# Kernel tuning notes

Hardware: AMD Instinct MI355X
Metric: run time of the kernel (lower is better)

Reference implementation:

```python
import jax, jax.numpy as jnp
import numpy as np

V, E, H, L = 32000, 512, 1024, 2
B, S, T = 32, 64, 64


def setup_inputs() -> dict:
    key = jax.random.key(0)
    ks = jax.random.split(key, 16)
    sd = 0.05
    p = lambda k, shape: (jax.random.normal(k, shape, jnp.float32) * sd)
    z = lambda shape: jnp.zeros(shape, jnp.float32)
    return {
        "tgt_batch": jax.random.randint(ks[0], (B, S), 0, V),
        "enc_h": p(ks[1], (L, B, H)),
        "enc_c": p(ks[2], (L, B, H)),
        "enc_outputs": p(ks[3], (T, B, H)),
        "emb": p(ks[4], (V, E)),
        "W_ih0": p(ks[5], (4 * H, E + H)),
        "W_hh0": p(ks[6], (4 * H, H)),
        "b_ih0": z((4 * H,)),
        "b_hh0": z((4 * H,)),
        "W_ih1": p(ks[7], (4 * H, H)),
        "W_hh1": p(ks[8], (4 * H, H)),
        "b_ih1": z((4 * H,)),
        "b_hh1": z((4 * H,)),
        "Wa": p(ks[9], (H, 2 * H)),
        "ba": z((H,)),
        "va": p(ks[10], (H,)),
        "Wc": p(ks[11], (H, 2 * H)),
        "bc": z((H,)),
        "Wo": p(ks[12], (V, H)),
        "bo": z((V,)),
        "teacher_forcing": 1,
    }


def _lstm_cell(x, h, c, Wih, Whh, bih, bhh):
    # PyTorch gate order: i, f, g, o
    g = x @ Wih.T + bih + h @ Whh.T + bhh
    i, f, gg, o = jnp.split(g, 4, axis=1)
    c2 = jax.nn.sigmoid(f) * c + jax.nn.sigmoid(i) * jnp.tanh(gg)
    return jax.nn.sigmoid(o) * jnp.tanh(c2), c2


def reference(tgt_batch, enc_h, enc_c, enc_outputs, emb,
              W_ih0, W_hh0, b_ih0, b_hh0, W_ih1, W_hh1, b_ih1, b_hh1,
              Wa, ba, va, Wc, bc, Wo, bo, teacher_forcing):
    # teacher_forcing == 1 -> always feed the gold previous word (matches
    # the torch loop, whose sampling branch is never taken at tf=1.0).
    tgt = tgt_batch.T  # [S, B], seq-first

    def step(carry, x_t):
        h, c, attn_h = carry  # h,c: [L,B,H]; attn_h: [B,H]
        x = jnp.concatenate([emb[x_t], attn_h], axis=1)  # [B, E+H]
        h0, c0 = _lstm_cell(x, h[0], c[0], W_ih0, W_hh0, b_ih0, b_hh0)
        h1, c1 = _lstm_cell(h0, h[1], c[1], W_ih1, W_hh1, b_ih1, b_hh1)
        # additive ('concat') attention over encoder states, query = top h
        hid = jnp.broadcast_to(h1[None], enc_outputs.shape)  # [T,B,H]
        energy = jnp.tanh(jnp.concatenate([hid, enc_outputs], axis=-1) @ Wa.T + ba)
        scores = jnp.einsum('tbh,h->bt', energy, va)  # [B,T]
        weights = jax.nn.softmax(scores, axis=1)
        context = jnp.einsum('bt,tbh->bh', weights, enc_outputs)  # [B,H]
        attn_h2 = jnp.tanh(jnp.concatenate([h1, context], axis=1) @ Wc.T + bc)
        logp = jax.nn.log_softmax(attn_h2 @ Wo.T + bo, axis=1)  # [B,V]
        return (jnp.stack([h0, h1]), jnp.stack([c0, c1]), attn_h2), logp

    init = (enc_h, enc_c, jnp.zeros((tgt.shape[1], H), enc_h.dtype))
    _, dec_outputs = jax.lax.scan(step, init, tgt[:-1])  # [S-1, B, V]
    dec_output_words = jnp.argmax(dec_outputs, axis=-1).astype(jnp.int32)
    return dec_outputs, dec_output_words
```

## Files before the change

### kernel.cpp

```cpp
#include <hip/hip_runtime.h>
#include <math.h>

#define VOCAB 32000
#define EMBD  512
#define HID   1024
#define BATCH 32
#define SEQ   64
#define TENC  64
#define NSTEP 63
#define G4    4096

typedef __attribute__((ext_vector_type(8))) short short8;
typedef __attribute__((ext_vector_type(4))) float f32x4;
typedef __attribute__((ext_vector_type(4))) unsigned short us4;
typedef unsigned short u16;

__device__ __forceinline__ float4 ld4(const float* p) {
  return *reinterpret_cast<const float4*>(p);
}
__device__ __forceinline__ u16 f2bf(float x) {
  unsigned u = __float_as_uint(x);
  return (u16)((u + 0x7fffu + ((u >> 16) & 1u)) >> 16);
}
__device__ __forceinline__ float bf2f(u16 h) {
  return __uint_as_float(((unsigned)h) << 16);
}

template<int MODE>
__device__ __forceinline__ void mfma32(
    const u16* __restrict__ Xahi, const u16* __restrict__ Xalo,
    const u16* __restrict__ Xbhi, const u16* __restrict__ Xblo,
    const u16* __restrict__ Whi,  const u16* __restrict__ Wlo,
    int nt, float* res)
{
  const int tid = threadIdx.x;
  const int w = tid >> 6, l = tid & 63;
  const int c = l & 15, koct = l >> 4;
  constexpr int K   = (MODE == 0) ? 2048 : 1024;
  constexpr int WS  = (MODE == 0) ? 2048 : 1024;
  constexpr int SPW = K / 32 / 4;
  const int r0 = c, r1 = 16 + c;
  const int wr0 = (MODE == 0) ? ((r0 >> 3)*1024 + nt*8 + (r0 & 7)) : (nt*32 + r0);
  const int wr1 = (MODE == 0) ? ((r1 >> 3)*1024 + nt*8 + (r1 & 7)) : (nt*32 + r1);
  const u16* bh0 = Whi + (size_t)wr0 * WS;
  const u16* bh1 = Whi + (size_t)wr1 * WS;
  const u16* bl0 = Wlo + (size_t)wr0 * WS;
  const u16* bl1 = Wlo + (size_t)wr1 * WS;

  auto ldA = [&](int m, int kg, int lo) -> short8 {
    const u16* base;
    if (MODE == 0 && kg >= 1024) base = lo ? Xblo : Xbhi;
    else                         base = lo ? Xalo : Xahi;
    const int b = m*16 + c;
    return *reinterpret_cast<const short8*>(base + b*1024 + (kg & 1023));
  };

  f32x4 acc[2][2];
  #pragma unroll
  for (int m = 0; m < 2; ++m)
    #pragma unroll
    for (int n = 0; n < 2; ++n) acc[m][n] = (f32x4){0.f,0.f,0.f,0.f};

  const int s0 = w * SPW;
  short8 Ah[2], Al[2], Bh[2], Bl[2];
  {
    const int kg = s0*32 + koct*8;
    Ah[0]=ldA(0,kg,0); Ah[1]=ldA(1,kg,0); Al[0]=ldA(0,kg,1); Al[1]=ldA(1,kg,1);
    Bh[0]=*reinterpret_cast<const short8*>(bh0+kg);
    Bh[1]=*reinterpret_cast<const short8*>(bh1+kg);
    Bl[0]=*reinterpret_cast<const short8*>(bl0+kg);
    Bl[1]=*reinterpret_cast<const short8*>(bl1+kg);
  }
  for (int s = s0; s < s0 + SPW; ++s) {
    short8 nAh[2], nAl[2], nBh[2], nBl[2];
    if (s + 1 < s0 + SPW) {
      const int kg = (s+1)*32 + koct*8;
      nAh[0]=ldA(0,kg,0); nAh[1]=ldA(1,kg,0); nAl[0]=ldA(0,kg,1); nAl[1]=ldA(1,kg,1);
      nBh[0]=*reinterpret_cast<const short8*>(bh0+kg);
      nBh[1]=*reinterpret_cast<const short8*>(bh1+kg);
      nBl[0]=*reinterpret_cast<const short8*>(bl0+kg);
      nBl[1]=*reinterpret_cast<const short8*>(bl1+kg);
    }
    #pragma unroll
    for (int n = 0; n < 2; ++n)
      #pragma unroll
      for (int m = 0; m < 2; ++m) {
        acc[m][n] = __builtin_amdgcn_mfma_f32_16x16x32_bf16(Ah[m], Bh[n], acc[m][n], 0, 0, 0);
        acc[m][n] = __builtin_amdgcn_mfma_f32_16x16x32_bf16(Ah[m], Bl[n], acc[m][n], 0, 0, 0);
        acc[m][n] = __builtin_amdgcn_mfma_f32_16x16x32_bf16(Al[m], Bh[n], acc[m][n], 0, 0, 0);
      }
    #pragma unroll
    for (int i = 0; i < 2; ++i) { Ah[i]=nAh[i]; Al[i]=nAl[i]; Bh[i]=nBh[i]; Bl[i]=nBl[i]; }
  }
  #pragma unroll
  for (int m = 0; m < 2; ++m)
    #pragma unroll
    for (int n = 0; n < 2; ++n)
      #pragma unroll
      for (int r = 0; r < 4; ++r) {
        const int b = m*16 + koct*4 + r;
        const int rr = n*16 + c;
        res[w*1056 + b*33 + rr] = acc[m][n][r];
      }
}

struct GKM {
  const u16 *Xahi, *Xalo, *Xbhi, *Xblo;
  const u16 *Whi, *Wlo;
  const float* bsum; const float* gembt;
  float* c; u16 *hhi; u16 *hlo;
};

template<int HASGEMB>
__global__ __launch_bounds__(256) void gates_mfma_k(GKM P) {
  __shared__ float res[4*1056];
  mfma32<0>(P.Xahi, P.Xalo, P.Xbhi, P.Xblo, P.Whi, P.Wlo, blockIdx.x, res);
  __syncthreads();
  const int tid = threadIdx.x;
  const int b = tid >> 3, j = tid & 7;
  const int n = blockIdx.x*8 + j;
  float g4[4];
  #pragma unroll
  for (int g = 0; g < 4; ++g) {
    const int r = g*8 + j;
    float s = P.bsum[g*1024 + n]
            + res[b*33+r] + res[1056 + b*33+r] + res[2112 + b*33+r] + res[3168 + b*33+r];
    if (HASGEMB) s += P.gembt[(size_t)b*G4 + g*1024 + n];
    g4[g] = s;
  }
  const float si = 1.f/(1.f+expf(-g4[0]));
  const float sf = 1.f/(1.f+expf(-g4[1]));
  const float so = 1.f/(1.f+expf(-g4[3]));
  const int i = b*HID + n;
  const float cn = sf*P.c[i] + si*tanhf(g4[2]);
  P.c[i] = cn;
  const float h = so*tanhf(cn);
  const u16 hh = f2bf(h);
  P.hhi[i] = hh;
  P.hlo[i] = f2bf(h - bf2f(hh));
}

struct PKM {
  const u16 *Xhi, *Xlo; const u16 *Whi, *Wlo; float* Pq;
};

__global__ __launch_bounds__(256) void proj_mfma_k(PKM P) {
  __shared__ float res[4*1056];
  mfma32<1>(P.Xhi, P.Xlo, nullptr, nullptr, P.Whi, P.Wlo, blockIdx.x, res);
  __syncthreads();
  const int tid = threadIdx.x;
  #pragma unroll
  for (int q = 0; q < 4; ++q) {
    const int o = q*256 + tid;
    const int b = o >> 5, r = o & 31;
    const float s = res[b*33+r] + res[1056 + b*33+r]
                  + res[2112 + b*33+r] + res[3168 + b*33+r];
    P.Pq[(size_t)b*2048 + blockIdx.x*32 + r] = s;
  }
}

struct AKM {
  const float* Pq; const float* PreAC; const float* va; const float* bc;
  u16* AHthi; u16* AHtlo;
};

__global__ __launch_bounds__(1024) void attn_k(AKM P) {
  __shared__ float QS[HID];
  __shared__ float sw[TENC];
  __shared__ float W64[TENC];
  const int b = blockIdx.x;
  const int tid = threadIdx.x;
  QS[tid] = P.Pq[(size_t)b*2048 + tid];
  __syncthreads();
  const int lane = tid & 63, wid = tid >> 6;
  float vreg[16];
  #pragma unroll
  for (int i2 = 0; i2 < 16; ++i2) vreg[i2] = P.va[lane + 64*i2];
  #pragma unroll
  for (int j = 0; j < 4; ++j) {
    const int te = wid*4 + j;
    const float* pr = P.PreAC + ((size_t)te*BATCH + b)*2048;
    float s = 0.f;
    #pragma unroll
    for (int i2 = 0; i2 < 16; ++i2) {
      const int idx = lane + 64*i2;
      s += vreg[i2] * tanhf(QS[idx] + pr[idx]);
    }
    #pragma unroll
    for (int off = 32; off; off >>= 1) s += __shfl_xor(s, off);
    if (lane == 0) sw[te] = s;
  }
  __syncthreads();
  if (tid < TENC) {
    const float v = sw[tid];
    float mx = v;
    #pragma unroll
    for (int off = 32; off; off >>= 1) mx = fmaxf(mx, __shfl_xor(mx, off));
    const float e = expf(v - mx);
    float sum = e;
    #pragma unroll
    for (int off = 32; off; off >>= 1) sum += __shfl_xor(sum, off);
    W64[tid] = e / sum;
  }
  __syncthreads();
  const int hh = tid;
  float acc = 0.f;
  #pragma unroll 8
  for (int te = 0; te < TENC; ++te)
    acc += W64[te] * P.PreAC[((size_t)te*BATCH + b)*2048 + HID + hh];
  const float hc = P.Pq[(size_t)b*2048 + HID + hh] + P.bc[hh];
  const float ah = tanhf(acc + hc);
  const u16 ahh = f2bf(ah);
  P.AHthi[(size_t)b*HID + hh] = ahh;
  P.AHtlo[(size_t)b*HID + hh] = f2bf(ah - bf2f(ahh));
}

template<int MODE>
__global__ __launch_bounds__(256) void pack_k(const float* __restrict__ A,
                                              const float* __restrict__ B,
                                              u16* __restrict__ hi, u16* __restrict__ lo) {
  constexpr int ROWS = (MODE == 2) ? 2048 : 4096;
  constexpr int K    = (MODE == 2) ? 1024 : 2048;
  const size_t total = (size_t)ROWS * (K/4);
  for (size_t i = (size_t)blockIdx.x*256 + threadIdx.x; i < total;
       i += (size_t)gridDim.x*256) {
    const int row = (int)(i / (K/4));
    const int k = (int)(i % (K/4)) * 4;
    float4 v;
    if (MODE == 0) v = (k < 1024) ? ld4(A + (size_t)row*1536 + 512 + k)
                                  : ld4(B + (size_t)row*1024 + (k - 1024));
    else if (MODE == 1) v = (k < 1024) ? ld4(A + (size_t)row*1024 + k)
                                       : ld4(B + (size_t)row*1024 + (k - 1024));
    else v = (row < 1024) ? ld4(A + (size_t)row*2048 + k)
                          : ld4(B + (size_t)(row - 1024)*2048 + k);
    us4 h, l;
    h.x = f2bf(v.x); l.x = f2bf(v.x - bf2f(h.x));
    h.y = f2bf(v.y); l.y = f2bf(v.y - bf2f(h.y));
    h.z = f2bf(v.z); l.z = f2bf(v.z - bf2f(h.z));
    h.w = f2bf(v.w); l.w = f2bf(v.w - bf2f(h.w));
    *reinterpret_cast<us4*>(hi + i*4) = h;
    *reinterpret_cast<us4*>(lo + i*4) = l;
  }
}

__global__ __launch_bounds__(256) void cvt_k(const float* __restrict__ src,
                                             u16* __restrict__ hi,
                                             u16* __restrict__ lo, int n) {
  int i = (blockIdx.x*256 + threadIdx.x) * 4;
  const int stride = gridDim.x * 256 * 4;
  for (; i < n; i += stride) {
    const float4 v = ld4(src + i);
    us4 h, l;
    h.x = f2bf(v.x); l.x = f2bf(v.x - bf2f(h.x));
    h.y = f2bf(v.y); l.y = f2bf(v.y - bf2f(h.y));
    h.z = f2bf(v.z); l.z = f2bf(v.z - bf2f(h.z));
    h.w = f2bf(v.w); l.w = f2bf(v.w - bf2f(h.w));
    *reinterpret_cast<us4*>(hi + i) = h;
    *reinterpret_cast<us4*>(lo + i) = l;
  }
}

struct WGP {
  const float* A; const float* W; const float* W2; const float* bias;
  const int* tgt; const float* emb;
  float* C; int ldc;
};

template<int WM>
__device__ __forceinline__ float4 ldWL(const WGP& P, int r, int k) {
  if (WM == 2) return ld4(P.W + (size_t)r * (EMBD + HID) + k);
  if (r < HID) return ld4(P.W  + (size_t)r * (2*HID) + HID + k);
  return ld4(P.W2 + (size_t)(r - HID) * (2*HID) + HID + k);
}

template<int WM>
__device__ __forceinline__ float4 ldAL(const WGP& P, int row, int k) {
  if (WM == 2) {
    const int tok = P.tgt[(row & 31) * SEQ + (row >> 5)];
    return ld4(P.emb + (size_t)tok * EMBD + k);
  }
  return ld4(P.A + (size_t)row * 1024 + k);
}

template<int WM>
__global__ __launch_bounds__(256, 2) void gemmL(WGP P) {
  constexpr int KK = (WM == 2) ? 512 : 1024;
  __shared__ float At[32*36];
  __shared__ float Wt[32*260];
  const int tid = threadIdx.x;
  const int m0 = blockIdx.x * 32;
  const int n0 = blockIdx.y * 256;
  const int lr = tid >> 3, lc = (tid & 7) << 2;
  const int tn = tid & 31, tm = tid >> 5;
  float acc[4][8];
  #pragma unroll
  for (int i = 0; i < 4; ++i)
    #pragma unroll
    for (int x = 0; x < 8; ++x) acc[i][x] = 0.f;

  float4 av = ldAL<WM>(P, m0 + lr, lc);
  float4 wv[8];
  #pragma unroll
  for (int it = 0; it < 8; ++it) wv[it] = ldWL<WM>(P, n0 + lr + it*32, lc);

  for (int k0 = 0; k0 < KK; k0 += 32) {
    float4 avn, wvn[8];
    if (k0 + 32 < KK) {
      avn = ldAL<WM>(P, m0 + lr, k0 + 32 + lc);
      #pragma unroll
      for (int it = 0; it < 8; ++it) wvn[it] = ldWL<WM>(P, n0 + lr + it*32, k0 + 32 + lc);
    }
    __syncthreads();
    At[(lc+0)*36+lr]=av.x; At[(lc+1)*36+lr]=av.y; At[(lc+2)*36+lr]=av.z; At[(lc+3)*36+lr]=av.w;
    #pragma unroll
    for (int it = 0; it < 8; ++it) {
      const int r = lr + it*32;
      Wt[(lc+0)*260+r]=wv[it].x; Wt[(lc+1)*260+r]=wv[it].y;
      Wt[(lc+2)*260+r]=wv[it].z; Wt[(lc+3)*260+r]=wv[it].w;
    }
    __syncthreads();
    #pragma unroll
    for (int kk = 0; kk < 32; ++kk) {
      const float4 a  = *reinterpret_cast<const float4*>(&At[kk*36 + tm*4]);
      const float4 w0 = *reinterpret_cast<const float4*>(&Wt[kk*260 + tn*8]);
      const float4 w1 = *reinterpret_cast<const float4*>(&Wt[kk*260 + tn*8 + 4]);
      #pragma unroll
      for (int i = 0; i < 4; ++i) {
        const float ai = (&a.x)[i];
        acc[i][0]+=ai*w0.x; acc[i][1]+=ai*w0.y; acc[i][2]+=ai*w0.z; acc[i][3]+=ai*w0.w;
        acc[i][4]+=ai*w1.x; acc[i][5]+=ai*w1.y; acc[i][6]+=ai*w1.z; acc[i][7]+=ai*w1.w;
      }
    }
    av = avn;
    #pragma unroll
    for (int it = 0; it < 8; ++it) wv[it] = wvn[it];
  }
  const int na = n0 + tn*8, ma = m0 + tm*4;
  float bb[8];
  #pragma unroll
  for (int x = 0; x < 8; ++x) {
    if (WM == 1) bb[x] = (na + x < HID) ? P.bias[na+x] : 0.f;
    else         bb[x] = 0.f;
  }
  #pragma unroll
  for (int i = 0; i < 4; ++i)
    #pragma unroll
    for (int x = 0; x < 8; ++x)
      P.C[(size_t)(ma+i)*P.ldc + na + x] = acc[i][x] + bb[x];
}

struct LM {
  const u16* Ahi; const u16* Alo;
  const u16* Bhi; const u16* Blo;
  const float* bo; float* out;
};

__global__ __launch_bounds__(256) void logits_mfma(LM P) {
  __shared__ u16 sA[2][4][64][8];
  __shared__ u16 sB[2][4][128][8];
  const int tid = threadIdx.x;
  const int m0 = blockIdx.x * 64;
  const int n0 = blockIdx.y * 128;
  const int w = tid >> 6, l = tid & 63;
  const int mb = (w & 1) * 32, nb = (w >> 1) * 64;
  f32x4 acc[2][4];
  #pragma unroll
  for (int mt = 0; mt < 2; ++mt)
    #pragma unroll
    for (int nt = 0; nt < 4; ++nt) acc[mt][nt] = (f32x4){0.f,0.f,0.f,0.f};

  const int arow = tid >> 2, akg = tid & 3;
  const int brow = tid >> 1, bkg = (tid & 1) * 2;
  short8 pah, pal, pbh0, pbh1, pbl0, pbl1;
  {
    const size_t ao = (size_t)(m0 + arow)*HID + akg*8;
    const size_t bo0 = (size_t)(n0 + brow)*HID + bkg*8;
    pah  = *reinterpret_cast<const short8*>(P.Ahi + ao);
    pal  = *reinterpret_cast<const short8*>(P.Alo + ao);
    pbh0 = *reinterpret_cast<const short8*>(P.Bhi + bo0);
    pbh1 = *reinterpret_cast<const short8*>(P.Bhi + bo0 + 8);
    pbl0 = *reinterpret_cast<const short8*>(P.Blo + bo0);
    pbl1 = *reinterpret_cast<const short8*>(P.Blo + bo0 + 8);
  }
  for (int kc = 0; kc < 32; ++kc) {
    __syncthreads();
    *reinterpret_cast<short8*>(&sA[0][akg][arow][0]) = pah;
    *reinterpret_cast<short8*>(&sA[1][akg][arow][0]) = pal;
    *reinterpret_cast<short8*>(&sB[0][bkg  ][brow][0]) = pbh0;
    *reinterpret_cast<short8*>(&sB[0][bkg+1][brow][0]) = pbh1;
    *reinterpret_cast<short8*>(&sB[1][bkg  ][brow][0]) = pbl0;
    *reinterpret_cast<short8*>(&sB[1][bkg+1][brow][0]) = pbl1;
    __syncthreads();
    if (kc + 1 < 32) {
      const size_t ao = (size_t)(m0 + arow)*HID + (kc+1)*32 + akg*8;
      const size_t bo0 = (size_t)(n0 + brow)*HID + (kc+1)*32 + bkg*8;
      pah  = *reinterpret_cast<const short8*>(P.Ahi + ao);
      pal  = *reinterpret_cast<const short8*>(P.Alo + ao);
      pbh0 = *reinterpret_cast<const short8*>(P.Bhi + bo0);
      pbh1 = *reinterpret_cast<const short8*>(P.Bhi + bo0 + 8);
      pbl0 = *reinterpret_cast<const short8*>(P.Blo + bo0);
      pbl1 = *reinterpret_cast<const short8*>(P.Blo + bo0 + 8);
    }
    const int kg = l >> 4, rr = l & 15;
    short8 ah[2], al[2];
    #pragma unroll
    for (int mt = 0; mt < 2; ++mt) {
      ah[mt] = *reinterpret_cast<const short8*>(&sA[0][kg][mb + mt*16 + rr][0]);
      al[mt] = *reinterpret_cast<const short8*>(&sA[1][kg][mb + mt*16 + rr][0]);
    }
    #pragma unroll
    for (int nt = 0; nt < 4; ++nt) {
      const short8 bh = *reinterpret_cast<const short8*>(&sB[0][kg][nb + nt*16 + rr][0]);
      const short8 bl = *reinterpret_cast<const short8*>(&sB[1][kg][nb + nt*16 + rr][0]);
      #pragma unroll
      for (int mt = 0; mt < 2; ++mt) {
        acc[mt][nt] = __builtin_amdgcn_mfma_f32_16x16x32_bf16(ah[mt], bh, acc[mt][nt], 0, 0, 0);
        acc[mt][nt] = __builtin_amdgcn_mfma_f32_16x16x32_bf16(ah[mt], bl, acc[mt][nt], 0, 0, 0);
        acc[mt][nt] = __builtin_amdgcn_mfma_f32_16x16x32_bf16(al[mt], bh, acc[mt][nt], 0, 0, 0);
      }
    }
  }
  #pragma unroll
  for (int mt = 0; mt < 2; ++mt) {
    #pragma unroll
    for (int nt = 0; nt < 4; ++nt) {
      #pragma unroll
      for (int r = 0; r < 4; ++r) {
        const int row = m0 + mb + mt*16 + (l >> 4)*4 + r;
        const int col = n0 + nb + nt*16 + (l & 15);
        if (row < NSTEP*BATCH)
          P.out[(size_t)row*VOCAB + col] = acc[mt][nt][r] + P.bo[col];
      }
    }
  }
}

__global__ __launch_bounds__(256) void lsm_k(float* __restrict__ out,
                                             float* __restrict__ words) {
  const int b = blockIdx.x;
  const int t = blockIdx.y;
  float* row = out + ((size_t)t*BATCH + b)*VOCAB;
  const int tid = threadIdx.x;
  float m = -INFINITY; int mi = 0;
  for (int v = tid; v < VOCAB; v += 256) {
    const float x = row[v];
    if (x > m) { m = x; mi = v; }
  }
  __shared__ float sm[256]; __shared__ int si[256];
  sm[tid] = m; si[tid] = mi;
  __syncthreads();
  for (int s2 = 128; s2; s2 >>= 1) {
    if (tid < s2) {
      const float om = sm[tid+s2]; const int oi = si[tid+s2];
      if (om > sm[tid] || (om == sm[tid] && oi < si[tid])) { sm[tid]=om; si[tid]=oi; }
    }
    __syncthreads();
  }
  const float mx = sm[0]; const int amax = si[0];
  float s = 0.f;
  for (int v = tid; v < VOCAB; v += 256) s += expf(row[v]-mx);
  __shared__ float ss[256];
  ss[tid] = s; __syncthreads();
  for (int s2=128; s2; s2>>=1) { if (tid < s2) ss[tid] += ss[tid+s2]; __syncthreads(); }
  const float lse = logf(ss[0]) + mx;
  for (int v = tid; v < VOCAB; v += 256) row[v] = row[v] - lse;
  if (tid == 0) words[(size_t)t*BATCH + b] = (float)amax;
}

__global__ __launch_bounds__(256) void init_k(const float* __restrict__ enc_h,
                                              const float* __restrict__ enc_c,
                                              const float* __restrict__ bih0,
                                              const float* __restrict__ bhh0,
                                              const float* __restrict__ bih1,
                                              const float* __restrict__ bhh1,
                                              float* c0, float* c1,
                                              u16* h0hi, u16* h0lo, u16* h1hi, u16* h1lo,
                                              u16* zahhi, u16* zahlo,
                                              float* bsum0, float* bsum1) {
  const int i = blockIdx.x*256 + threadIdx.x;
  if (i < BATCH*HID) {
    c0[i] = enc_c[i]; c1[i] = enc_c[BATCH*HID + i];
    const float v0 = enc_h[i];
    const u16 h0 = f2bf(v0);
    h0hi[i] = h0; h0lo[i] = f2bf(v0 - bf2f(h0));
    const float v1 = enc_h[BATCH*HID + i];
    const u16 h1 = f2bf(v1);
    h1hi[i] = h1; h1lo[i] = f2bf(v1 - bf2f(h1));
    zahhi[i] = 0; zahlo[i] = 0;
  }
  if (i < G4) {
    bsum0[i] = bih0[i] + bhh0[i];
    bsum1[i] = bih1[i] + bhh1[i];
  }
}

extern "C" void kernel_launch(void* const* d_in, const int* in_sizes, int n_in,
                              void* d_out, int out_size, void* d_ws, size_t ws_size,
                              hipStream_t stream) {
  const int*   tgt   = (const int*)d_in[0];
  const float* enc_h = (const float*)d_in[1];
  const float* enc_c = (const float*)d_in[2];
  const float* enc   = (const float*)d_in[3];
  const float* emb   = (const float*)d_in[4];
  const float* Wih0  = (const float*)d_in[5];
  const float* Whh0  = (const float*)d_in[6];
  const float* bih0  = (const float*)d_in[7];
  const float* bhh0  = (const float*)d_in[8];
  const float* Wih1  = (const float*)d_in[9];
  const float* Whh1  = (const float*)d_in[10];
  const float* bih1  = (const float*)d_in[11];
  const float* bhh1  = (const float*)d_in[12];
  const float* Wa    = (const float*)d_in[13];
  const float* ba    = (const float*)d_in[14];
  const float* va    = (const float*)d_in[15];
  const float* Wc    = (const float*)d_in[16];
  const float* bc    = (const float*)d_in[17];
  const float* Wo    = (const float*)d_in[18];
  const float* bo    = (const float*)d_in[19];

  u16* AHhi = (u16*)d_ws;
  u16* AHlo = AHhi + (size_t)2048*1024;
  float* pool = (float*)(AHlo + (size_t)2048*1024);

  float* PreAC = pool;
  float* Gemb  = PreAC + (size_t)2048*2048;
  float* Pq    = Gemb  + (size_t)NSTEP*BATCH*G4;
  float* c0    = Pq    + (size_t)BATCH*2048;
  float* c1v   = c0    + BATCH*HID;
  float* bsum0 = c1v   + BATCH*HID;
  float* bsum1 = bsum0 + G4;
  u16* W0hi = (u16*)(bsum1 + G4);
  u16* W0lo = W0hi + (size_t)4096*2048;
  u16* W1hi = W0lo + (size_t)4096*2048;
  u16* W1lo = W1hi + (size_t)4096*2048;
  u16* WAhi = W1lo + (size_t)4096*2048;
  u16* WAlo = WAhi + (size_t)2048*1024;
  u16* h0Ahi = WAlo + (size_t)2048*1024;
  u16* h0Alo = h0Ahi + BATCH*HID;
  u16* h0Bhi = h0Alo + BATCH*HID;
  u16* h0Blo = h0Bhi + BATCH*HID;
  u16* h1Ahi = h0Blo + BATCH*HID;
  u16* h1Alo = h1Ahi + BATCH*HID;
  u16* h1Bhi = h1Alo + BATCH*HID;
  u16* h1Blo = h1Bhi + BATCH*HID;
  u16* zahhi = h1Blo + BATCH*HID;
  u16* zahlo = zahhi + BATCH*HID;
  u16* Wohi = (u16*)pool;
  u16* Wolo = Wohi + (size_t)VOCAB*1024;

  float* out   = (float*)d_out;
  float* words = out + (size_t)NSTEP*BATCH*VOCAB;

  init_k<<<dim3(128), 256, 0, stream>>>(enc_h, enc_c, bih0, bhh0, bih1, bhh1,
                                        c0, c1v, h0Ahi, h0Alo, h1Ahi, h1Alo,
                                        zahhi, zahlo, bsum0, bsum1);

  {
    WGP p = {}; p.A = enc; p.W = Wa; p.W2 = Wc; p.bias = ba; p.C = PreAC; p.ldc = 2048;
    gemmL<1><<<dim3(64, 8), 256, 0, stream>>>(p);
  }
  {
    WGP p = {}; p.W = Wih0; p.tgt = tgt; p.emb = emb; p.C = Gemb; p.ldc = G4;
    gemmL<2><<<dim3(NSTEP*BATCH/32, G4/256), 256, 0, stream>>>(p);
  }
  pack_k<0><<<dim3(1024), 256, 0, stream>>>(Wih0, Whh0, W0hi, W0lo);
  pack_k<1><<<dim3(1024), 256, 0, stream>>>(Wih1, Whh1, W1hi, W1lo);
  pack_k<2><<<dim3(512), 256, 0, stream>>>(Wa, Wc, WAhi, WAlo);

  for (int t = 0; t < NSTEP; ++t) {
    const u16* ahphi = t ? (AHhi + (size_t)(t-1)*BATCH*HID) : zahhi;
    const u16* ahplo = t ? (AHlo + (size_t)(t-1)*BATCH*HID) : zahlo;
    const u16* h0phi = (t & 1) ? h0Bhi : h0Ahi;
    const u16* h0plo = (t & 1) ? h0Blo : h0Alo;
    u16* h0chi = (t & 1) ? h0Ahi : h0Bhi;
    u16* h0clo = (t & 1) ? h0Alo : h0Blo;
    const u16* h1phi = (t & 1) ? h1Bhi : h1Ahi;
    const u16* h1plo = (t & 1) ? h1Blo : h1Alo;
    u16* h1chi = (t & 1) ? h1Ahi : h1Bhi;
    u16* h1clo = (t & 1) ? h1Alo : h1Blo;

    {
      GKM p = {};
      p.Xahi = ahphi; p.Xalo = ahplo; p.Xbhi = h0phi; p.Xblo = h0plo;
      p.Whi = W0hi; p.Wlo = W0lo;
      p.bsum = bsum0; p.gembt = Gemb + (size_t)t*BATCH*G4;
      p.c = c0; p.hhi = h0chi; p.hlo = h0clo;
      gates_mfma_k<1><<<dim3(128), 256, 0, stream>>>(p);
    }
    {
      GKM p = {};
      p.Xahi = h0chi; p.Xalo = h0clo; p.Xbhi = h1phi; p.Xblo = h1plo;
      p.Whi = W1hi; p.Wlo = W1lo;
      p.bsum = bsum1; p.gembt = nullptr;
      p.c = c1v; p.hhi = h1chi; p.hlo = h1clo;
      gates_mfma_k<0><<<dim3(128), 256, 0, stream>>>(p);
    }
    {
      PKM p; p.Xhi = h1chi; p.Xlo = h1clo; p.Whi = WAhi; p.Wlo = WAlo; p.Pq = Pq;
      proj_mfma_k<<<dim3(64), 256, 0, stream>>>(p);
    }
    {
      AKM p; p.Pq = Pq; p.PreAC = PreAC; p.va = va; p.bc = bc;
      p.AHthi = AHhi + (size_t)t*BATCH*HID;
      p.AHtlo = AHlo + (size_t)t*BATCH*HID;
      attn_k<<<dim3(BATCH), 1024, 0, stream>>>(p);
    }
  }

  cvt_k<<<dim3(4096), 256, 0, stream>>>(Wo, Wohi, Wolo, VOCAB*1024);
  {
    LM p; p.Ahi = AHhi; p.Alo = AHlo; p.Bhi = Wohi; p.Blo = Wolo;
    p.bo = bo; p.out = out;
    logits_mfma<<<dim3(32, VOCAB/128), 256, 0, stream>>>(p);
  }
  lsm_k<<<dim3(BATCH, NSTEP), 256, 0, stream>>>(out, words);
}
```

Before: 5.914 ms.

## Interleave output-projection logits tiles into idle CUs of recurrent step kernels

Each recurrent-step launch (gates, proj, attn) now gets up to 32 extra blocks. These compute 64x128 tiles of the vocabulary logits GEMM for timesteps whose attention outputs are already finished. This uses CUs that sit idle during the latency-bound sequential loop instead of running the whole logits GEMM afterwards. Wo is converted to bf16 hi/lo before the loop into a separate workspace region, which requires enough workspace and otherwise falls back to the old path. The attention kernel moves from 1024 to 256 threads to share the block shape. The risk is that the extra tile blocks lengthen every critical-path launch.

```diff
diff --git a/kernel.cpp b/kernel.cpp
--- a/kernel.cpp
+++ b/kernel.cpp
@@ -9,6 +9,8 @@
 #define TENC  64
 #define NSTEP 63
 #define G4    4096
+#define NTILE_N 250
+#define NTILES  8000
 
 typedef __attribute__((ext_vector_type(8))) short short8;
 typedef __attribute__((ext_vector_type(4))) float f32x4;
@@ -24,6 +26,97 @@
 }
 __device__ __forceinline__ float bf2f(u16 h) {
   return __uint_as_float(((unsigned)h) << 16);
+}
+
+struct LM {
+  const u16* Ahi; const u16* Alo;
+  const u16* Bhi; const u16* Blo;
+  const float* bo; float* out;
+};
+
+__device__ void logits_tile(const LM& P, int tile, float* smemf) {
+  u16* sA = (u16*)smemf;
+  u16* sB = sA + 4096;
+  const int mi = tile / NTILE_N, ni = tile % NTILE_N;
+  const int m0 = mi * 64, n0 = ni * 128;
+  const int tid = threadIdx.x;
+  const int w = tid >> 6, l = tid & 63;
+  const int mb = (w & 1) * 32, nb = (w >> 1) * 64;
+  f32x4 acc[2][4];
+  #pragma unroll
+  for (int mt = 0; mt < 2; ++mt)
+    #pragma unroll
+    for (int nt = 0; nt < 4; ++nt) acc[mt][nt] = (f32x4){0.f,0.f,0.f,0.f};
+
+  const int arow = tid >> 2, akg = tid & 3;
+  const int brow = tid >> 1, bkg = (tid & 1) * 2;
+  short8 pah, pal, pbh0, pbh1, pbl0, pbl1;
+  {
+    const size_t ao = (size_t)(m0 + arow)*HID + akg*8;
+    const size_t bo0 = (size_t)(n0 + brow)*HID + bkg*8;
+    pah  = *reinterpret_cast<const short8*>(P.Ahi + ao);
+    pal  = *reinterpret_cast<const short8*>(P.Alo + ao);
+    pbh0 = *reinterpret_cast<const short8*>(P.Bhi + bo0);
+    pbh1 = *reinterpret_cast<const short8*>(P.Bhi + bo0 + 8);
+    pbl0 = *reinterpret_cast<const short8*>(P.Blo + bo0);
+    pbl1 = *reinterpret_cast<const short8*>(P.Blo + bo0 + 8);
+  }
+  for (int kc = 0; kc < 32; ++kc) {
+    __syncthreads();
+    *reinterpret_cast<short8*>(sA + ((0*4 + akg)*64 + arow)*8) = pah;
+    *reinterpret_cast<short8*>(sA + ((1*4 + akg)*64 + arow)*8) = pal;
+    *reinterpret_cast<short8*>(sB + ((0*4 + bkg  )*128 + brow)*8) = pbh0;
+    *reinterpret_cast<short8*>(sB + ((0*4 + bkg+1)*128 + brow)*8) = pbh1;
+    *reinterpret_cast<short8*>(sB + ((1*4 + bkg  )*128 + brow)*8) = pbl0;
+    *reinterpret_cast<short8*>(sB + ((1*4 + bkg+1)*128 + brow)*8) = pbl1;
+    __syncthreads();
+    if (kc + 1 < 32) {
+      const size_t ao = (size_t)(m0 + arow)*HID + (kc+1)*32 + akg*8;
+      const size_t bo0 = (size_t)(n0 + brow)*HID + (kc+1)*32 + bkg*8;
+      pah  = *reinterpret_cast<const short8*>(P.Ahi + ao);
+      pal  = *reinterpret_cast<const short8*>(P.Alo + ao);
+      pbh0 = *reinterpret_cast<const short8*>(P.Bhi + bo0);
+      pbh1 = *reinterpret_cast<const short8*>(P.Bhi + bo0 + 8);
+      pbl0 = *reinterpret_cast<const short8*>(P.Blo + bo0);
+      pbl1 = *reinterpret_cast<const short8*>(P.Blo + bo0 + 8);
+    }
+    const int kg = l >> 4, rr = l & 15;
+    short8 ah[2], al[2];
+    #pragma unroll
+    for (int mt = 0; mt < 2; ++mt) {
+      ah[mt] = *reinterpret_cast<const short8*>(sA + ((0*4 + kg)*64 + mb + mt*16 + rr)*8);
+      al[mt] = *reinterpret_cast<const short8*>(sA + ((1*4 + kg)*64 + mb + mt*16 + rr)*8);
+    }
+    #pragma unroll
+    for (int nt = 0; nt < 4; ++nt) {
+      const short8 bh = *reinterpret_cast<const short8*>(sB + ((0*4 + kg)*128 + nb + nt*16 + rr)*8);
+      const short8 bl = *reinterpret_cast<const short8*>(sB + ((1*4 + kg)*128 + nb + nt*16 + rr)*8);
+      #pragma unroll
+      for (int mt = 0; mt < 2; ++mt) {
+        acc[mt][nt] = __builtin_amdgcn_mfma_f32_16x16x32_bf16(ah[mt], bh, acc[mt][nt], 0, 0, 0);
+        acc[mt][nt] = __builtin_amdgcn_mfma_f32_16x16x32_bf16(ah[mt], bl, acc[mt][nt], 0, 0, 0);
+        acc[mt][nt] = __builtin_amdgcn_mfma_f32_16x16x32_bf16(al[mt], bh, acc[mt][nt], 0, 0, 0);
+      }
+    }
+  }
+  #pragma unroll
+  for (int mt = 0; mt < 2; ++mt) {
+    #pragma unroll
+    for (int nt = 0; nt < 4; ++nt) {
+      #pragma unroll
+      for (int r = 0; r < 4; ++r) {
+        const int row = m0 + mb + mt*16 + (l >> 4)*4 + r;
+        const int col = n0 + nb + nt*16 + (l & 15);
+        if (row < NSTEP*BATCH)
+          P.out[(size_t)row*VOCAB + col] = acc[mt][nt][r] + P.bo[col];
+      }
+    }
+  }
+}
+
+__global__ __launch_bounds__(256) void logits_tiles_k(LM P, int qbase) {
+  __shared__ float smem[6144];
+  logits_tile(P, qbase + blockIdx.x, smem);
 }
 
 template<int MODE>
@@ -109,11 +202,18 @@
   const u16 *Whi, *Wlo;
   const float* bsum; const float* gembt;
   float* c; u16 *hhi; u16 *hlo;
+  LM lm; int qbase, qcount;
 };
 
 template<int HASGEMB>
 __global__ __launch_bounds__(256) void gates_mfma_k(GKM P) {
-  __shared__ float res[4*1056];
+  __shared__ float smem[6144];
+  if (blockIdx.x >= 128) {
+    const int e = blockIdx.x - 128;
+    if (e < P.qcount) logits_tile(P.lm, P.qbase + e, smem);
+    return;
+  }
+  float* res = smem;
   mfma32<0>(P.Xahi, P.Xalo, P.Xbhi, P.Xblo, P.Whi, P.Wlo, blockIdx.x, res);
   __syncthreads();
   const int tid = threadIdx.x;
@@ -142,10 +242,17 @@
 
 struct PKM {
   const u16 *Xhi, *Xlo; const u16 *Whi, *Wlo; float* Pq;
+  LM lm; int qbase, qcount;
 };
 
 __global__ __launch_bounds__(256) void proj_mfma_k(PKM P) {
-  __shared__ float res[4*1056];
+  __shared__ float smem[6144];
+  if (blockIdx.x >= 64) {
+    const int e = blockIdx.x - 64;
+    if (e < P.qcount) logits_tile(P.lm, P.qbase + e, smem);
+    return;
+  }
+  float* res = smem;
   mfma32<1>(P.Xhi, P.Xlo, nullptr, nullptr, P.Whi, P.Wlo, blockIdx.x, res);
   __syncthreads();
   const int tid = threadIdx.x;
@@ -162,23 +269,31 @@
 struct AKM {
   const float* Pq; const float* PreAC; const float* va; const float* bc;
   u16* AHthi; u16* AHtlo;
+  LM lm; int qbase, qcount;
 };
 
-__global__ __launch_bounds__(1024) void attn_k(AKM P) {
-  __shared__ float QS[HID];
-  __shared__ float sw[TENC];
-  __shared__ float W64[TENC];
+__global__ __launch_bounds__(256) void attn_k(AKM P) {
+  __shared__ float smem[6144];
+  if (blockIdx.x >= 32) {
+    const int e = blockIdx.x - 32;
+    if (e < P.qcount) logits_tile(P.lm, P.qbase + e, smem);
+    return;
+  }
+  float* QS  = smem;
+  float* sw  = smem + 1024;
+  float* W64 = smem + 1088;
   const int b = blockIdx.x;
   const int tid = threadIdx.x;
-  QS[tid] = P.Pq[(size_t)b*2048 + tid];
+  #pragma unroll
+  for (int q = 0; q < 4; ++q) QS[q*256 + tid] = P.Pq[(size_t)b*2048 + q*256 + tid];
   __syncthreads();
   const int lane = tid & 63, wid = tid >> 6;
   float vreg[16];
   #pragma unroll
   for (int i2 = 0; i2 < 16; ++i2) vreg[i2] = P.va[lane + 64*i2];
   #pragma unroll
-  for (int j = 0; j < 4; ++j) {
-    const int te = wid*4 + j;
+  for (int j = 0; j < 16; ++j) {
+    const int te = wid*16 + j;
     const float* pr = P.PreAC + ((size_t)te*BATCH + b)*2048;
     float s = 0.f;
     #pragma unroll
@@ -203,16 +318,19 @@
     W64[tid] = e / sum;
   }
   __syncthreads();
-  const int hh = tid;
-  float acc = 0.f;
-  #pragma unroll 8
-  for (int te = 0; te < TENC; ++te)
-    acc += W64[te] * P.PreAC[((size_t)te*BATCH + b)*2048 + HID + hh];
-  const float hc = P.Pq[(size_t)b*2048 + HID + hh] + P.bc[hh];
-  const float ah = tanhf(acc + hc);
-  const u16 ahh = f2bf(ah);
-  P.AHthi[(size_t)b*HID + hh] = ahh;
-  P.AHtlo[(size_t)b*HID + hh] = f2bf(ah - bf2f(ahh));
+  #pragma unroll
+  for (int q = 0; q < 4; ++q) {
+    const int hh = q*256 + tid;
+    float acc = 0.f;
+    #pragma unroll 8
+    for (int te = 0; te < TENC; ++te)
+      acc += W64[te] * P.PreAC[((size_t)te*BATCH + b)*2048 + HID + hh];
+    const float hc = P.Pq[(size_t)b*2048 + HID + hh] + P.bc[hh];
+    const float ah = tanhf(acc + hc);
+    const u16 ahh = f2bf(ah);
+    P.AHthi[(size_t)b*HID + hh] = ahh;
+    P.AHtlo[(size_t)b*HID + hh] = f2bf(ah - bf2f(ahh));
+  }
 }
 
 template<int MODE>
@@ -349,92 +467,6 @@
       P.C[(size_t)(ma+i)*P.ldc + na + x] = acc[i][x] + bb[x];
 }
 
-struct LM {
-  const u16* Ahi; const u16* Alo;
-  const u16* Bhi; const u16* Blo;
-  const float* bo; float* out;
-};
-
-__global__ __launch_bounds__(256) void logits_mfma(LM P) {
-  __shared__ u16 sA[2][4][64][8];
-  __shared__ u16 sB[2][4][128][8];
-  const int tid = threadIdx.x;
-  const int m0 = blockIdx.x * 64;
-  const int n0 = blockIdx.y * 128;
-  const int w = tid >> 6, l = tid & 63;
-  const int mb = (w & 1) * 32, nb = (w >> 1) * 64;
-  f32x4 acc[2][4];
-  #pragma unroll
-  for (int mt = 0; mt < 2; ++mt)
-    #pragma unroll
-    for (int nt = 0; nt < 4; ++nt) acc[mt][nt] = (f32x4){0.f,0.f,0.f,0.f};
-
-  const int arow = tid >> 2, akg = tid & 3;
-  const int brow = tid >> 1, bkg = (tid & 1) * 2;
-  short8 pah, pal, pbh0, pbh1, pbl0, pbl1;
-  {
-    const size_t ao = (size_t)(m0 + arow)*HID + akg*8;
-    const size_t bo0 = (size_t)(n0 + brow)*HID + bkg*8;
-    pah  = *reinterpret_cast<const short8*>(P.Ahi + ao);
-    pal  = *reinterpret_cast<const short8*>(P.Alo + ao);
-    pbh0 = *reinterpret_cast<const short8*>(P.Bhi + bo0);
-    pbh1 = *reinterpret_cast<const short8*>(P.Bhi + bo0 + 8);
-    pbl0 = *reinterpret_cast<const short8*>(P.Blo + bo0);
-    pbl1 = *reinterpret_cast<const short8*>(P.Blo + bo0 + 8);
-  }
-  for (int kc = 0; kc < 32; ++kc) {
-    __syncthreads();
-    *reinterpret_cast<short8*>(&sA[0][akg][arow][0]) = pah;
-    *reinterpret_cast<short8*>(&sA[1][akg][arow][0]) = pal;
-    *reinterpret_cast<short8*>(&sB[0][bkg  ][brow][0]) = pbh0;
-    *reinterpret_cast<short8*>(&sB[0][bkg+1][brow][0]) = pbh1;
-    *reinterpret_cast<short8*>(&sB[1][bkg  ][brow][0]) = pbl0;
-    *reinterpret_cast<short8*>(&sB[1][bkg+1][brow][0]) = pbl1;
-    __syncthreads();
-    if (kc + 1 < 32) {
-      const size_t ao = (size_t)(m0 + arow)*HID + (kc+1)*32 + akg*8;
-      const size_t bo0 = (size_t)(n0 + brow)*HID + (kc+1)*32 + bkg*8;
-      pah  = *reinterpret_cast<const short8*>(P.Ahi + ao);
-      pal  = *reinterpret_cast<const short8*>(P.Alo + ao);
-      pbh0 = *reinterpret_cast<const short8*>(P.Bhi + bo0);
-      pbh1 = *reinterpret_cast<const short8*>(P.Bhi + bo0 + 8);
-      pbl0 = *reinterpret_cast<const short8*>(P.Blo + bo0);
-      pbl1 = *reinterpret_cast<const short8*>(P.Blo + bo0 + 8);
-    }
-    const int kg = l >> 4, rr = l & 15;
-    short8 ah[2], al[2];
-    #pragma unroll
-    for (int mt = 0; mt < 2; ++mt) {
-      ah[mt] = *reinterpret_cast<const short8*>(&sA[0][kg][mb + mt*16 + rr][0]);
-      al[mt] = *reinterpret_cast<const short8*>(&sA[1][kg][mb + mt*16 + rr][0]);
-    }
-    #pragma unroll
-    for (int nt = 0; nt < 4; ++nt) {
-      const short8 bh = *reinterpret_cast<const short8*>(&sB[0][kg][nb + nt*16 + rr][0]);
-      const short8 bl = *reinterpret_cast<const short8*>(&sB[1][kg][nb + nt*16 + rr][0]);
-      #pragma unroll
-      for (int mt = 0; mt < 2; ++mt) {
-        acc[mt][nt] = __builtin_amdgcn_mfma_f32_16x16x32_bf16(ah[mt], bh, acc[mt][nt], 0, 0, 0);
-        acc[mt][nt] = __builtin_amdgcn_mfma_f32_16x16x32_bf16(ah[mt], bl, acc[mt][nt], 0, 0, 0);
-        acc[mt][nt] = __builtin_amdgcn_mfma_f32_16x16x32_bf16(al[mt], bh, acc[mt][nt], 0, 0, 0);
-      }
-    }
-  }
-  #pragma unroll
-  for (int mt = 0; mt < 2; ++mt) {
-    #pragma unroll
-    for (int nt = 0; nt < 4; ++nt) {
-      #pragma unroll
-      for (int r = 0; r < 4; ++r) {
-        const int row = m0 + mb + mt*16 + (l >> 4)*4 + r;
-        const int col = n0 + nb + nt*16 + (l & 15);
-        if (row < NSTEP*BATCH)
-          P.out[(size_t)row*VOCAB + col] = acc[mt][nt][r] + P.bo[col];
-      }
-    }
-  }
-}
-
 __global__ __launch_bounds__(256) void lsm_k(float* __restrict__ out,
                                              float* __restrict__ words) {
   const int b = blockIdx.x;
@@ -518,35 +550,44 @@
   const float* Wo    = (const float*)d_in[18];
   const float* bo    = (const float*)d_in[19];
 
-  u16* AHhi = (u16*)d_ws;
-  u16* AHlo = AHhi + (size_t)2048*1024;
-  float* pool = (float*)(AHlo + (size_t)2048*1024);
-
-  float* PreAC = pool;
-  float* Gemb  = PreAC + (size_t)2048*2048;
-  float* Pq    = Gemb  + (size_t)NSTEP*BATCH*G4;
-  float* c0    = Pq    + (size_t)BATCH*2048;
-  float* c1v   = c0    + BATCH*HID;
-  float* bsum0 = c1v   + BATCH*HID;
-  float* bsum1 = bsum0 + G4;
-  u16* W0hi = (u16*)(bsum1 + G4);
-  u16* W0lo = W0hi + (size_t)4096*2048;
-  u16* W1hi = W0lo + (size_t)4096*2048;
-  u16* W1lo = W1hi + (size_t)4096*2048;
-  u16* WAhi = W1lo + (size_t)4096*2048;
-  u16* WAlo = WAhi + (size_t)2048*1024;
-  u16* h0Ahi = WAlo + (size_t)2048*1024;
-  u16* h0Alo = h0Ahi + BATCH*HID;
-  u16* h0Bhi = h0Alo + BATCH*HID;
-  u16* h0Blo = h0Bhi + BATCH*HID;
-  u16* h1Ahi = h0Blo + BATCH*HID;
-  u16* h1Alo = h1Ahi + BATCH*HID;
-  u16* h1Bhi = h1Alo + BATCH*HID;
-  u16* h1Blo = h1Bhi + BATCH*HID;
-  u16* zahhi = h1Blo + BATCH*HID;
-  u16* zahlo = zahhi + BATCH*HID;
-  u16* Wohi = (u16*)pool;
-  u16* Wolo = Wohi + (size_t)VOCAB*1024;
+  char* base = (char*)d_ws;
+  size_t cur = 0;
+  auto take = [&](size_t bytes) { char* p = base + cur; cur = (cur + bytes + 63) & ~(size_t)63; return p; };
+
+  u16* AHhi = (u16*)take((size_t)2048*1024*2);
+  u16* AHlo = (u16*)take((size_t)2048*1024*2);
+  float* PreAC = (float*)take((size_t)2048*2048*4);
+  float* Gemb  = (float*)take((size_t)NSTEP*BATCH*G4*4);
+  float* Pq    = (float*)take((size_t)BATCH*2048*4);
+  float* c0    = (float*)take(BATCH*HID*4);
+  float* c1v   = (float*)take(BATCH*HID*4);
+  float* bsum0 = (float*)take(G4*4);
+  float* bsum1 = (float*)take(G4*4);
+  u16* W0hi = (u16*)take((size_t)4096*2048*2);
+  u16* W0lo = (u16*)take((size_t)4096*2048*2);
+  u16* W1hi = (u16*)take((size_t)4096*2048*2);
+  u16* W1lo = (u16*)take((size_t)4096*2048*2);
+  u16* WAhi = (u16*)take((size_t)2048*1024*2);
+  u16* WAlo = (u16*)take((size_t)2048*1024*2);
+  u16* h0Ahi = (u16*)take(BATCH*HID*2);
+  u16* h0Alo = (u16*)take(BATCH*HID*2);
+  u16* h0Bhi = (u16*)take(BATCH*HID*2);
+  u16* h0Blo = (u16*)take(BATCH*HID*2);
+  u16* h1Ahi = (u16*)take(BATCH*HID*2);
+  u16* h1Alo = (u16*)take(BATCH*HID*2);
+  u16* h1Bhi = (u16*)take(BATCH*HID*2);
+  u16* h1Blo = (u16*)take(BATCH*HID*2);
+  u16* zahhi = (u16*)take(BATCH*HID*2);
+  u16* zahlo = (u16*)take(BATCH*HID*2);
+  const size_t loop_end = cur;
+  u16* Wohi_i = (u16*)take((size_t)VOCAB*1024*2);
+  u16* Wolo_i = (u16*)take((size_t)VOCAB*1024*2);
+  const bool interleave = ws_size >= cur;
+  u16* Wohi_f = (u16*)PreAC;
+  u16* Wolo_f = Wohi_f + (size_t)VOCAB*1024;
+  u16* Wohi = interleave ? Wohi_i : Wohi_f;
+  u16* Wolo = interleave ? Wolo_i : Wolo_f;
+  (void)loop_end;
 
   float* out   = (float*)d_out;
   float* words = out + (size_t)NSTEP*BATCH*VOCAB;
@@ -566,6 +607,21 @@
   pack_k<0><<<dim3(1024), 256, 0, stream>>>(Wih0, Whh0, W0hi, W0lo);
   pack_k<1><<<dim3(1024), 256, 0, stream>>>(Wih1, Whh1, W1hi, W1lo);
   pack_k<2><<<dim3(512), 256, 0, stream>>>(Wa, Wc, WAhi, WAlo);
+  if (interleave)
+    cvt_k<<<dim3(4096), 256, 0, stream>>>(Wo, Wohi, Wolo, VOCAB*1024);
+
+  LM lm; lm.Ahi = AHhi; lm.Alo = AHlo; lm.Bhi = Wohi; lm.Blo = Wolo;
+  lm.bo = bo; lm.out = out;
+
+  int qpos = 0;
+  auto next_q = [&](int t) -> int {
+    if (!interleave) return 0;
+    const int avail = (t < 2) ? 0 : NTILE_N * (t / 2);
+    int n = avail - qpos;
+    if (n > 32) n = 32;
+    if (n < 0) n = 0;
+    return n;
+  };
 
   for (int t = 0; t < NSTEP; ++t) {
     const u16* ahphi = t ? (AHhi + (size_t)(t-1)*BATCH*HID) : zahhi;
@@ -585,7 +641,8 @@
       p.Whi = W0hi; p.Wlo = W0lo;
       p.bsum = bsum0; p.gembt = Gemb + (size_t)t*BATCH*G4;
       p.c = c0; p.hhi = h0chi; p.hlo = h0clo;
-      gates_mfma_k<1><<<dim3(128), 256, 0, stream>>>(p);
+      p.lm = lm; p.qbase = qpos; p.qcount = next_q(t); qpos += p.qcount;
+      gates_mfma_k<1><<<dim3(128 + p.qcount), 256, 0, stream>>>(p);
     }
     {
       GKM p = {};
@@ -593,25 +650,28 @@
       p.Whi = W1hi; p.Wlo = W1lo;
       p.bsum = bsum1; p.gembt = nullptr;
       p.c = c1v; p.hhi = h1chi; p.hlo = h1clo;
-      gates_mfma_k<0><<<dim3(128), 256, 0, stream>>>(p);
+      p.lm = lm; p.qbase = qpos; p.qcount = next_q(t); qpos += p.qcount;
+      gates_mfma_k<0><<<dim3(128 + p.qcount), 256, 0, stream>>>(p);
     }
     {
-      PKM p; p.Xhi = h1chi; p.Xlo = h1clo; p.Whi = WAhi; p.Wlo = WAlo; p.Pq = Pq;
-      proj_mfma_k<<<dim3(64), 256, 0, stream>>>(p);
+      PKM p = {};
+      p.Xhi = h1chi; p.Xlo = h1clo; p.Whi = WAhi; p.Wlo = WAlo; p.Pq = Pq;
+      p.lm = lm; p.qbase = qpos; p.qcount = next_q(t); qpos += p.qcount;
+      proj_mfma_k<<<dim3(64 + p.qcount), 256, 0, stream>>>(p);
     }
     {
-      AKM p; p.Pq = Pq; p.PreAC = PreAC; p.va = va; p.bc = bc;
+      AKM p = {};
+      p.Pq = Pq; p.PreAC = PreAC; p.va = va; p.bc = bc;
       p.AHthi = AHhi + (size_t)t*BATCH*HID;
       p.AHtlo = AHlo + (size_t)t*BATCH*HID;
-      attn_k<<<dim3(BATCH), 1024, 0, stream>>>(p);
-    }
-  }
-
-  cvt_k<<<dim3(4096), 256, 0, stream>>>(Wo, Wohi, Wolo, VOCAB*1024);
-  {
-    LM p; p.Ahi = AHhi; p.Alo = AHlo; p.Bhi = Wohi; p.Blo = Wolo;
-    p.bo = bo; p.out = out;
-    logits_mfma<<<dim3(32, VOCAB/128), 256, 0, stream>>>(p);
-  }
+      p.lm = lm; p.qbase = qpos; p.qcount = next_q(t); qpos += p.qcount;
+      attn_k<<<dim3(32 + p.qcount), 256, 0, stream>>>(p);
+    }
+  }
+
+  if (!interleave)
+    cvt_k<<<dim3(4096), 256, 0, stream>>>(Wo, Wohi, Wolo, VOCAB*1024);
+  if (qpos < NTILES)
+    logits_tiles_k<<<dim3(NTILES - qpos), 256, 0, stream>>>(lm, qpos);
   lsm_k<<<dim3(BATCH, NSTEP), 256, 0, stream>>>(out, words);
 }
```

Result: slower. 12.60 ms (+113.0%).
